# Performance work log

Measured on AMD Instinct MI355X. Metric: run time of the kernel, lower is better.

Reference implementation:

```python
import jax, jax.numpy as jnp
import numpy as np

FLOW_ITERS = 8
DUAL_ITERS = 8
DUAL_STEP = 0.1
DUAL_MOM = 0.9
GRAPH_LAYERS = 2
BIG = 1e9


def _sparsemax(z, mask):
    # sparsemax along last axis; masked entries already hold -BIG, zeroed by mask after.
    V = z.shape[-1]
    zs = jnp.sort(z, axis=-1)[..., ::-1]
    cum = jnp.cumsum(zs, axis=-1)
    k = jnp.arange(1, V + 1, dtype=z.dtype)
    support = zs * k > (cum - 1.0)
    k_sel = jnp.sum(support.astype(jnp.int32), axis=-1, keepdims=True)
    tau = (jnp.take_along_axis(cum, k_sel - 1, axis=-1) - 1.0) / k_sel.astype(z.dtype)
    return jnp.maximum(z - tau, 0.0) * mask


def _min_cost_flow(props, demands):
    # iterative proportional flow routing: push relu(inflow - demand) along predicted proportions
    def body(flow, _):
        inflow = jnp.sum(flow, axis=1)[..., None]      # [B,V,1] inflow to each node
        adjusted = jax.nn.relu(inflow - demands)       # excess to re-route
        return props * adjusted, None                  # row i scaled by its excess
    flow0 = jnp.zeros_like(props)
    flow, _ = jax.lax.scan(body, flow0, None, length=FLOW_ITERS)
    return flow


def _dual_flow(dual_diff, adj):
    # Nesterov-momentum projected gradient on cost(x)=x^2 minus linear dual term, x>=0 on edges
    def body(carry, _):
        flow, acc = carry
        look = flow - DUAL_MOM * acc
        grad = 2.0 * look - dual_diff                  # d/dx x^2 - dual_diff
        acc = DUAL_MOM * acc + DUAL_STEP * grad
        flow = adj * jax.nn.relu(flow - acc)
        return (flow, acc), None
    z = jnp.zeros_like(dual_diff)
    (flow, _), _ = jax.lax.scan(body, (z, z), None, length=DUAL_ITERS)
    return flow


def setup_inputs():
    key = jax.random.key(0)
    ks = jax.random.split(key, 32)
    B, V, F, E, D, K, H = 8, 1200, 8, 16, 64, 2, 4
    node_features = jax.random.normal(ks[0], (B, V, F), dtype=jnp.float32)
    node_embeddings = jax.random.normal(ks[1], (B, V, E), dtype=jnp.float32)
    d = jax.random.normal(ks[2], (B, V, 1), dtype=jnp.float32)
    demands = d - jnp.mean(d, axis=1, keepdims=True)   # balanced supply/demand per graph
    eye = jnp.eye(V, dtype=jnp.float32)
    adj = (jax.random.uniform(ks[3], (B, V, V)) < (16.0 / V)).astype(jnp.float32) * (1.0 - eye)
    hop2 = jnp.clip(adj @ adj, 0.0, 1.0) * (1.0 - eye)
    neighborhoods = jnp.stack([adj, hop2], axis=0)     # [K,B,V,V] k-hop neighborhoods

    def dense(k, fin, fout):
        return (jax.random.normal(k, (fin, fout), dtype=jnp.float32) / np.sqrt(fin)).astype(jnp.float32)

    return dict(
        node_features=node_features, node_embeddings=node_embeddings,
        demands=demands, adj=adj, neighborhoods=neighborhoods,
        enc_w0=dense(ks[4], E + F, D), enc_b0=jnp.zeros((D,), jnp.float32),
        enc_w1=dense(ks[5], D, D), enc_b1=jnp.zeros((D,), jnp.float32),
        agg_w=(jax.random.normal(ks[6], (K, D, D)) / np.sqrt(D)).astype(jnp.float32),
        agg_b=jnp.zeros((K, D), jnp.float32),
        att_w=(jax.random.normal(ks[7], (H, D, D)) / np.sqrt(D)).astype(jnp.float32),
        att_b=jnp.zeros((H, D), jnp.float32),
        att_v=(jax.random.normal(ks[8], (H, D)) / np.sqrt(D)).astype(jnp.float32),
        gru_wu=dense(ks[9], 2 * D, D), gru_bu=jnp.zeros((D,), jnp.float32),
        gru_wr=dense(ks[10], 2 * D, D), gru_br=jnp.zeros((D,), jnp.float32),
        gru_wc=dense(ks[11], 2 * D, D), gru_bc=jnp.zeros((D,), jnp.float32),
        dec_w0=dense(ks[12], D, D), dec_b0=jnp.zeros((D,), jnp.float32),
        dec_w1=dense(ks[13], D, 1), dec_b1=jnp.zeros((1,), jnp.float32),
        dual_w0=dense(ks[14], D, D), dual_b0=jnp.zeros((D,), jnp.float32),
        dual_w1=dense(ks[15], D, 1), dual_b1=jnp.zeros((1,), jnp.float32),
    )


def reference(node_features, node_embeddings, demands, adj, neighborhoods,
              enc_w0, enc_b0, enc_w1, enc_b1, agg_w, agg_b, att_w, att_b, att_v,
              gru_wu, gru_bu, gru_wr, gru_br, gru_wc, gru_bc,
              dec_w0, dec_b0, dec_w1, dec_b1, dual_w0, dual_b0, dual_w1, dual_b1):
    H = att_w.shape[0]
    # node encoder MLP (tanh hidden, tanh final since activate_final=True)
    x = jnp.concatenate([node_embeddings, node_features], axis=-1)
    enc = jnp.tanh(jnp.tanh(x @ enc_w0 + enc_b0) @ enc_w1 + enc_b1)            # [B,V,D]

    deg = jnp.sum(neighborhoods, axis=-1, keepdims=True)
    nb_norm = neighborhoods / jnp.maximum(deg, 1.0)                            # [K,B,V,V]

    for _ in range(GRAPH_LAYERS):
        # per-hop neighborhood aggregation
        msg = jnp.einsum('kbuv,bvd->kbud', nb_norm, enc)
        agg = jnp.tanh(jnp.einsum('kbud,kde->kbue', msg, agg_w) + agg_b[:, None, None, :])
        # multi-head attention over the K hop levels
        proj = jnp.tanh(jnp.einsum('kbvd,hde->hkbve', agg, att_w) + att_b[:, None, None, None, :])
        scores = jnp.einsum('hkbve,he->hkbv', proj, att_v)
        attn = jax.nn.softmax(scores, axis=1)                                  # softmax over hops
        nxt = jnp.einsum('hkbv,kbvd->bvd', attn, agg) / H                      # mean over heads
        # GRU state update
        xs = jnp.concatenate([nxt, enc], axis=-1)
        u = jax.nn.sigmoid(xs @ gru_wu + gru_bu)
        r = jax.nn.sigmoid(xs @ gru_wr + gru_br)
        c = jnp.tanh(jnp.concatenate([nxt, r * enc], axis=-1) @ gru_wc + gru_bc)
        enc = u * enc + (1.0 - u) * c

    # primal: edge weights -> sparsemax -> min-cost-flow
    pred = (enc @ dec_w0 + dec_b0) @ dec_w1 + dec_b1                           # [B,V,1]
    pred_weights = adj * jnp.transpose(pred, (0, 2, 1))                        # [B,V,V]
    weights = -BIG * (1.0 - adj) + pred_weights
    flow_props = _sparsemax(weights, adj)
    flow = _min_cost_flow(flow_props, demands)
    flow_cost = jnp.sum(flow * flow, axis=(1, 2))                              # square cost

    # dual: potentials -> dual-diff -> dual flow solver
    dual = (enc @ dual_w0 + dual_b0) @ dual_w1 + dual_b1                       # [B,V,1]
    dual_diff = adj * (dual - jnp.transpose(dual, (0, 2, 1)))
    dflow = _dual_flow(dual_diff, adj)
    dual_demand = jnp.sum(dual * demands, axis=(1, 2))
    dual_cost = jnp.sum(dflow * dflow - dual_diff * dflow, axis=(1, 2)) - dual_demand

    return flow_cost - dual_cost                                               # duality-gap loss, [B]
```

## Files before the change

### kernel.cpp

```cpp
#include <hip/hip_runtime.h>

#define BB 8
#define VV 1200
#define DD 64
#define KH 2
#define NH 4
#define CAP 64
#define NB2CAP 384
#define NROW (BB*VV)
#define NKROW (KH*BB*VV)

__device__ __forceinline__ float wredsum(float v) {
#pragma unroll
  for (int o = 32; o > 0; o >>= 1) v += __shfl_xor(v, o, 64);
  return v;
}
__device__ __forceinline__ float gredsum(float v) {
#pragma unroll
  for (int o = 8; o > 0; o >>= 1) v += __shfl_xor(v, o, 64);
  return v;
}

__device__ __forceinline__ float tanh_f(float x) {
  float e = __expf(2.0f * x);
  return 1.0f - 2.0f / (e + 1.0f);
}
__device__ __forceinline__ float sigmoid_f(float x) { return 1.0f / (1.0f + __expf(-x)); }

__device__ __forceinline__ size_t nb_base(int row) {
  return (row < NROW) ? (size_t)row * CAP
                      : (size_t)NROW * CAP + (size_t)(row - NROW) * NB2CAP;
}

__global__ void __launch_bounds__(256) k_nbcsr(
    const float* __restrict__ nb,
    int* __restrict__ nb_cols, int* __restrict__ nb_cnt) {
  int wid = threadIdx.x >> 6, lane = threadIdx.x & 63;
  int row = blockIdx.x * 4 + wid;
  if (row >= NKROW) return;
  const float* nbrow = nb + (size_t)row * VV;
  size_t base = nb_base(row);
  int cap = (row < NROW) ? CAP : NB2CAP;
  unsigned long long ltmask = (lane == 0) ? 0ull : ((1ull << lane) - 1ull);
  int cnt = 0;
  for (int b0 = 0; b0 < VV; b0 += 64) {
    int v = b0 + lane;
    float val = (v < VV) ? nbrow[v] : 0.0f;
    unsigned long long mask = __ballot(val != 0.0f);
    int off = cnt + __popcll(mask & ltmask);
    if (val != 0.0f && off < cap) nb_cols[base + off] = v;
    cnt += __popcll(mask);
  }
  if (lane == 0) nb_cnt[row] = (cnt > cap) ? cap : cnt;
}

__global__ void __launch_bounds__(256) k_encoder(
    const float* __restrict__ emb, const float* __restrict__ feat,
    const float* __restrict__ w0, const float* __restrict__ b0,
    const float* __restrict__ w1, const float* __restrict__ b1,
    float* __restrict__ enc0) {
  __shared__ float xT[8][25];
  __shared__ float hT[8][65];
  int tid = threadIdx.x;
  int tile0 = blockIdx.x * 8;
  if (tid < 128) { int i = tid >> 4, d = tid & 15; xT[i][d] = emb[(size_t)(tile0 + i) * 16 + d]; }
  else if (tid < 192) { int t = tid - 128; int i = t >> 3, d = t & 7; xT[i][16 + d] = feat[(size_t)(tile0 + i) * 8 + d]; }
  __syncthreads();
  int r = tid >> 5, cg = tid & 31;
  int c0 = cg * 2;
  float a0 = b0[c0], a1 = b0[c0 + 1];
#pragma unroll
  for (int kk = 0; kk < 24; ++kk) {
    float x = xT[r][kk];
    float2 w2 = *(const float2*)(w0 + kk * DD + c0);
    a0 = fmaf(x, w2.x, a0); a1 = fmaf(x, w2.y, a1);
  }
  hT[r][c0] = tanh_f(a0); hT[r][c0 + 1] = tanh_f(a1);
  __syncthreads();
  float g0 = b1[c0], g1 = b1[c0 + 1];
#pragma unroll 16
  for (int kk = 0; kk < DD; ++kk) {
    float x = hT[r][kk];
    float2 w2 = *(const float2*)(w1 + kk * DD + c0);
    g0 = fmaf(x, w2.x, g0); g1 = fmaf(x, w2.y, g1);
  }
  float2 o; o.x = tanh_f(g0); o.y = tanh_f(g1);
  *(float2*)(enc0 + (size_t)(tile0 + r) * DD + c0) = o;
}

__global__ void __launch_bounds__(256) k_gather(
    const int* __restrict__ nb_cols, const int* __restrict__ nb_cnt,
    const float* __restrict__ encIn, float* __restrict__ msg) {
  int w = threadIdx.x >> 6, lane = threadIdx.x & 63;
  int row = blockIdx.x * 4 + w;
  int k = (row >= NROW) ? 1 : 0;
  int bv = row - k * NROW;
  int b = bv / VV;
  const float4* enc4 = (const float4*)(encIn + (size_t)b * VV * DD);
  const int* cols = nb_cols + nb_base(row);
  int n = nb_cnt[row];
  int sub = lane >> 4, q = lane & 15;
  float ax = 0.0f, ay = 0.0f, az = 0.0f, aw = 0.0f;
  int j = 0;
  for (; j + 16 <= n; j += 16) {
    int c0 = cols[j + sub];
    int c1 = cols[j + 4 + sub];
    int c2 = cols[j + 8 + sub];
    int c3 = cols[j + 12 + sub];
    float4 v0 = enc4[(size_t)c0 * 16 + q];
    float4 v1 = enc4[(size_t)c1 * 16 + q];
    float4 v2 = enc4[(size_t)c2 * 16 + q];
    float4 v3 = enc4[(size_t)c3 * 16 + q];
    ax += (v0.x + v1.x) + (v2.x + v3.x);
    ay += (v0.y + v1.y) + (v2.y + v3.y);
    az += (v0.z + v1.z) + (v2.z + v3.z);
    aw += (v0.w + v1.w) + (v2.w + v3.w);
  }
  for (; j < n; j += 4) {
    int idx = j + sub;
    if (idx < n) {
      float4 v = enc4[(size_t)cols[idx] * 16 + q];
      ax += v.x; ay += v.y; az += v.z; aw += v.w;
    }
  }
#pragma unroll
  for (int o = 16; o < 64; o <<= 1) {
    ax += __shfl_xor(ax, o, 64);
    ay += __shfl_xor(ay, o, 64);
    az += __shfl_xor(az, o, 64);
    aw += __shfl_xor(aw, o, 64);
  }
  if (lane < 16) {
    float inv = 1.0f / fmaxf((float)n, 1.0f);
    float4 r; r.x = ax * inv; r.y = ay * inv; r.z = az * inv; r.w = aw * inv;
    ((float4*)(msg + (size_t)row * DD))[q] = r;
  }
}

__global__ void __launch_bounds__(256) k_aggatt(
    const float* __restrict__ msg,
    const float* __restrict__ agg_w, const float* __restrict__ agg_b,
    const float* __restrict__ att_w, const float* __restrict__ att_b,
    const float* __restrict__ att_v,
    float* __restrict__ agg, float* __restrict__ scores) {
  __shared__ float M[64][65];
  __shared__ float G[64][65];
  int tid = threadIdx.x;
  int tile0 = blockIdx.x * 64;
  int k = (tile0 >= NROW) ? 1 : 0;
  int bv0 = tile0 - k * NROW;
  int rsub = tid >> 4, cg = tid & 15;
  int c0 = cg * 4;
  int r0 = rsub * 4;
#pragma unroll
  for (int rep = 0; rep < 4; ++rep) {
    int idx = rep * 256 + tid; int i = idx >> 4, d4 = idx & 15;
    float4 m4 = *(const float4*)(msg + (size_t)(tile0 + i) * DD + d4 * 4);
    M[i][d4 * 4] = m4.x; M[i][d4 * 4 + 1] = m4.y; M[i][d4 * 4 + 2] = m4.z; M[i][d4 * 4 + 3] = m4.w;
  }
  __syncthreads();
  const float* W = agg_w + (size_t)k * DD * DD;
  float acc[4][4];
#pragma unroll
  for (int i = 0; i < 4; ++i)
#pragma unroll
    for (int j = 0; j < 4; ++j) acc[i][j] = agg_b[k * DD + c0 + j];
#pragma unroll 4
  for (int kk = 0; kk < DD; ++kk) {
    float4 w4 = *(const float4*)(W + kk * DD + c0);
    float x0 = M[r0][kk], x1 = M[r0 + 1][kk], x2 = M[r0 + 2][kk], x3 = M[r0 + 3][kk];
    acc[0][0] = fmaf(x0, w4.x, acc[0][0]); acc[0][1] = fmaf(x0, w4.y, acc[0][1]);
    acc[0][2] = fmaf(x0, w4.z, acc[0][2]); acc[0][3] = fmaf(x0, w4.w, acc[0][3]);
    acc[1][0] = fmaf(x1, w4.x, acc[1][0]); acc[1][1] = fmaf(x1, w4.y, acc[1][1]);
    acc[1][2] = fmaf(x1, w4.z, acc[1][2]); acc[1][3] = fmaf(x1, w4.w, acc[1][3]);
    acc[2][0] = fmaf(x2, w4.x, acc[2][0]); acc[2][1] = fmaf(x2, w4.y, acc[2][1]);
    acc[2][2] = fmaf(x2, w4.z, acc[2][2]); acc[2][3] = fmaf(x2, w4.w, acc[2][3]);
    acc[3][0] = fmaf(x3, w4.x, acc[3][0]); acc[3][1] = fmaf(x3, w4.y, acc[3][1]);
    acc[3][2] = fmaf(x3, w4.z, acc[3][2]); acc[3][3] = fmaf(x3, w4.w, acc[3][3]);
  }
#pragma unroll
  for (int i = 0; i < 4; ++i) {
    float4 g4;
    g4.x = tanh_f(acc[i][0]); g4.y = tanh_f(acc[i][1]);
    g4.z = tanh_f(acc[i][2]); g4.w = tanh_f(acc[i][3]);
    G[r0 + i][c0] = g4.x; G[r0 + i][c0 + 1] = g4.y; G[r0 + i][c0 + 2] = g4.z; G[r0 + i][c0 + 3] = g4.w;
    *(float4*)(agg + (size_t)(tile0 + r0 + i) * DD + c0) = g4;
  }
  __syncthreads();
#pragma unroll
  for (int h = 0; h < NH; ++h) {
    const float* Wh = att_w + (size_t)h * DD * DD;
    float a2[4][4];
#pragma unroll
    for (int i = 0; i < 4; ++i)
#pragma unroll
      for (int j = 0; j < 4; ++j) a2[i][j] = att_b[h * DD + c0 + j];
#pragma unroll 4
    for (int kk = 0; kk < DD; ++kk) {
      float4 w4 = *(const float4*)(Wh + kk * DD + c0);
      float x0 = G[r0][kk], x1 = G[r0 + 1][kk], x2 = G[r0 + 2][kk], x3 = G[r0 + 3][kk];
      a2[0][0] = fmaf(x0, w4.x, a2[0][0]); a2[0][1] = fmaf(x0, w4.y, a2[0][1]);
      a2[0][2] = fmaf(x0, w4.z, a2[0][2]); a2[0][3] = fmaf(x0, w4.w, a2[0][3]);
      a2[1][0] = fmaf(x1, w4.x, a2[1][0]); a2[1][1] = fmaf(x1, w4.y, a2[1][1]);
      a2[1][2] = fmaf(x1, w4.z, a2[1][2]); a2[1][3] = fmaf(x1, w4.w, a2[1][3]);
      a2[2][0] = fmaf(x2, w4.x, a2[2][0]); a2[2][1] = fmaf(x2, w4.y, a2[2][1]);
      a2[2][2] = fmaf(x2, w4.z, a2[2][2]); a2[2][3] = fmaf(x2, w4.w, a2[2][3]);
      a2[3][0] = fmaf(x3, w4.x, a2[3][0]); a2[3][1] = fmaf(x3, w4.y, a2[3][1]);
      a2[3][2] = fmaf(x3, w4.z, a2[3][2]); a2[3][3] = fmaf(x3, w4.w, a2[3][3]);
    }
    float4 v4 = *(const float4*)(att_v + h * DD + c0);
#pragma unroll
    for (int i = 0; i < 4; ++i) {
      float p = tanh_f(a2[i][0]) * v4.x + tanh_f(a2[i][1]) * v4.y
              + tanh_f(a2[i][2]) * v4.z + tanh_f(a2[i][3]) * v4.w;
      p = gredsum(p);
      if (cg == 0) scores[(size_t)(h * KH + k) * NROW + bv0 + r0 + i] = p;
    }
  }
}

__global__ void __launch_bounds__(256) k_gru(
    const float* __restrict__ encIn, const float* __restrict__ agg,
    const float* __restrict__ scores,
    const float* __restrict__ wu, const float* __restrict__ bu,
    const float* __restrict__ wr, const float* __restrict__ br,
    const float* __restrict__ wc, const float* __restrict__ bc,
    float* __restrict__ encOut,
    int do_decode,
    const float* __restrict__ dw0, const float* __restrict__ db0,
    const float* __restrict__ dw1, const float* __restrict__ db1,
    const float* __restrict__ uw0, const float* __restrict__ ub0,
    const float* __restrict__ uw1, const float* __restrict__ ub1,
    float* __restrict__ pred, float* __restrict__ dualp) {
  __shared__ float X[64][129];
  __shared__ float EO[64][65];
  __shared__ float wmix[2][64];
  int tid = threadIdx.x;
  int tile0 = blockIdx.x * 64;
  int rsub = tid >> 4, cg = tid & 15;
  int c0 = cg * 4;
  int r0 = rsub * 4;
  if (tid < 64) {
    int row = tile0 + tid;
    float W0 = 0.0f, W1 = 0.0f;
#pragma unroll
    for (int h = 0; h < NH; ++h) {
      float s0 = scores[(size_t)(h * KH + 0) * NROW + row];
      float s1 = scores[(size_t)(h * KH + 1) * NROW + row];
      float m = fmaxf(s0, s1);
      float e0 = __expf(s0 - m), e1 = __expf(s1 - m);
      float inv = 1.0f / (e0 + e1);
      W0 += e0 * inv; W1 += e1 * inv;
    }
    wmix[0][tid] = W0 * 0.25f;
    wmix[1][tid] = W1 * 0.25f;
  }
  __syncthreads();
#pragma unroll
  for (int rep = 0; rep < 4; ++rep) {
    int idx = rep * 256 + tid; int i = idx >> 4, d4 = idx & 15;
    float4 e4 = *(const float4*)(encIn + (size_t)(tile0 + i) * DD + d4 * 4);
    float4 a0 = *(const float4*)(agg + (size_t)(tile0 + i) * DD + d4 * 4);
    float4 a1 = *(const float4*)(agg + (size_t)(NROW + tile0 + i) * DD + d4 * 4);
    float m0 = wmix[0][i], m1 = wmix[1][i];
    X[i][d4 * 4]     = m0 * a0.x + m1 * a1.x;
    X[i][d4 * 4 + 1] = m0 * a0.y + m1 * a1.y;
    X[i][d4 * 4 + 2] = m0 * a0.z + m1 * a1.z;
    X[i][d4 * 4 + 3] = m0 * a0.w + m1 * a1.w;
    X[i][64 + d4 * 4]     = e4.x;
    X[i][64 + d4 * 4 + 1] = e4.y;
    X[i][64 + d4 * 4 + 2] = e4.z;
    X[i][64 + d4 * 4 + 3] = e4.w;
  }
  __syncthreads();
  float au[4][4], ar[4][4];
#pragma unroll
  for (int i = 0; i < 4; ++i)
#pragma unroll
    for (int j = 0; j < 4; ++j) { au[i][j] = bu[c0 + j]; ar[i][j] = br[c0 + j]; }
#pragma unroll 4
  for (int kk = 0; kk < 2 * DD; ++kk) {
    float4 u4 = *(const float4*)(wu + kk * DD + c0);
    float4 r4 = *(const float4*)(wr + kk * DD + c0);
    float x0 = X[r0][kk], x1 = X[r0 + 1][kk], x2 = X[r0 + 2][kk], x3 = X[r0 + 3][kk];
    au[0][0] = fmaf(x0, u4.x, au[0][0]); au[0][1] = fmaf(x0, u4.y, au[0][1]);
    au[0][2] = fmaf(x0, u4.z, au[0][2]); au[0][3] = fmaf(x0, u4.w, au[0][3]);
    au[1][0] = fmaf(x1, u4.x, au[1][0]); au[1][1] = fmaf(x1, u4.y, au[1][1]);
    au[1][2] = fmaf(x1, u4.z, au[1][2]); au[1][3] = fmaf(x1, u4.w, au[1][3]);
    au[2][0] = fmaf(x2, u4.x, au[2][0]); au[2][1] = fmaf(x2, u4.y, au[2][1]);
    au[2][2] = fmaf(x2, u4.z, au[2][2]); au[2][3] = fmaf(x2, u4.w, au[2][3]);
    au[3][0] = fmaf(x3, u4.x, au[3][0]); au[3][1] = fmaf(x3, u4.y, au[3][1]);
    au[3][2] = fmaf(x3, u4.z, au[3][2]); au[3][3] = fmaf(x3, u4.w, au[3][3]);
    ar[0][0] = fmaf(x0, r4.x, ar[0][0]); ar[0][1] = fmaf(x0, r4.y, ar[0][1]);
    ar[0][2] = fmaf(x0, r4.z, ar[0][2]); ar[0][3] = fmaf(x0, r4.w, ar[0][3]);
    ar[1][0] = fmaf(x1, r4.x, ar[1][0]); ar[1][1] = fmaf(x1, r4.y, ar[1][1]);
    ar[1][2] = fmaf(x1, r4.z, ar[1][2]); ar[1][3] = fmaf(x1, r4.w, ar[1][3]);
    ar[2][0] = fmaf(x2, r4.x, ar[2][0]); ar[2][1] = fmaf(x2, r4.y, ar[2][1]);
    ar[2][2] = fmaf(x2, r4.z, ar[2][2]); ar[2][3] = fmaf(x2, r4.w, ar[2][3]);
    ar[3][0] = fmaf(x3, r4.x, ar[3][0]); ar[3][1] = fmaf(x3, r4.y, ar[3][1]);
    ar[3][2] = fmaf(x3, r4.z, ar[3][2]); ar[3][3] = fmaf(x3, r4.w, ar[3][3]);
  }
  float uu[4][4], encv[4][4];
#pragma unroll
  for (int i = 0; i < 4; ++i)
#pragma unroll
    for (int j = 0; j < 4; ++j) {
      uu[i][j] = sigmoid_f(au[i][j]);
      encv[i][j] = X[r0 + i][64 + c0 + j];
    }
  __syncthreads();
#pragma unroll
  for (int i = 0; i < 4; ++i)
#pragma unroll
    for (int j = 0; j < 4; ++j)
      X[r0 + i][64 + c0 + j] = encv[i][j] * sigmoid_f(ar[i][j]);
  __syncthreads();
  float ac[4][4];
#pragma unroll
  for (int i = 0; i < 4; ++i)
#pragma unroll
    for (int j = 0; j < 4; ++j) ac[i][j] = bc[c0 + j];
#pragma unroll 4
  for (int kk = 0; kk < 2 * DD; ++kk) {
    float4 c4 = *(const float4*)(wc + kk * DD + c0);
    float x0 = X[r0][kk], x1 = X[r0 + 1][kk], x2 = X[r0 + 2][kk], x3 = X[r0 + 3][kk];
    ac[0][0] = fmaf(x0, c4.x, ac[0][0]); ac[0][1] = fmaf(x0, c4.y, ac[0][1]);
    ac[0][2] = fmaf(x0, c4.z, ac[0][2]); ac[0][3] = fmaf(x0, c4.w, ac[0][3]);
    ac[1][0] = fmaf(x1, c4.x, ac[1][0]); ac[1][1] = fmaf(x1, c4.y, ac[1][1]);
    ac[1][2] = fmaf(x1, c4.z, ac[1][2]); ac[1][3] = fmaf(x1, c4.w, ac[1][3]);
    ac[2][0] = fmaf(x2, c4.x, ac[2][0]); ac[2][1] = fmaf(x2, c4.y, ac[2][1]);
    ac[2][2] = fmaf(x2, c4.z, ac[2][2]); ac[2][3] = fmaf(x2, c4.w, ac[2][3]);
    ac[3][0] = fmaf(x3, c4.x, ac[3][0]); ac[3][1] = fmaf(x3, c4.y, ac[3][1]);
    ac[3][2] = fmaf(x3, c4.z, ac[3][2]); ac[3][3] = fmaf(x3, c4.w, ac[3][3]);
  }
#pragma unroll
  for (int i = 0; i < 4; ++i) {
    float4 e4;
    e4.x = uu[i][0] * encv[i][0] + (1.0f - uu[i][0]) * tanh_f(ac[i][0]);
    e4.y = uu[i][1] * encv[i][1] + (1.0f - uu[i][1]) * tanh_f(ac[i][1]);
    e4.z = uu[i][2] * encv[i][2] + (1.0f - uu[i][2]) * tanh_f(ac[i][2]);
    e4.w = uu[i][3] * encv[i][3] + (1.0f - uu[i][3]) * tanh_f(ac[i][3]);
    *(float4*)(encOut + (size_t)(tile0 + r0 + i) * DD + c0) = e4;
    EO[r0 + i][c0] = e4.x; EO[r0 + i][c0 + 1] = e4.y;
    EO[r0 + i][c0 + 2] = e4.z; EO[r0 + i][c0 + 3] = e4.w;
  }
  if (do_decode) {
    __syncthreads();
    float hd[4][4], hq[4][4];
#pragma unroll
    for (int i = 0; i < 4; ++i)
#pragma unroll
      for (int j = 0; j < 4; ++j) { hd[i][j] = db0[c0 + j]; hq[i][j] = ub0[c0 + j]; }
#pragma unroll 4
    for (int kk = 0; kk < DD; ++kk) {
      float4 d4 = *(const float4*)(dw0 + kk * DD + c0);
      float4 q4 = *(const float4*)(uw0 + kk * DD + c0);
      float x0 = EO[r0][kk], x1 = EO[r0 + 1][kk], x2 = EO[r0 + 2][kk], x3 = EO[r0 + 3][kk];
      hd[0][0] = fmaf(x0, d4.x, hd[0][0]); hd[0][1] = fmaf(x0, d4.y, hd[0][1]);
      hd[0][2] = fmaf(x0, d4.z, hd[0][2]); hd[0][3] = fmaf(x0, d4.w, hd[0][3]);
      hd[1][0] = fmaf(x1, d4.x, hd[1][0]); hd[1][1] = fmaf(x1, d4.y, hd[1][1]);
      hd[1][2] = fmaf(x1, d4.z, hd[1][2]); hd[1][3] = fmaf(x1, d4.w, hd[1][3]);
      hd[2][0] = fmaf(x2, d4.x, hd[2][0]); hd[2][1] = fmaf(x2, d4.y, hd[2][1]);
      hd[2][2] = fmaf(x2, d4.z, hd[2][2]); hd[2][3] = fmaf(x2, d4.w, hd[2][3]);
      hd[3][0] = fmaf(x3, d4.x, hd[3][0]); hd[3][1] = fmaf(x3, d4.y, hd[3][1]);
      hd[3][2] = fmaf(x3, d4.z, hd[3][2]); hd[3][3] = fmaf(x3, d4.w, hd[3][3]);
      hq[0][0] = fmaf(x0, q4.x, hq[0][0]); hq[0][1] = fmaf(x0, q4.y, hq[0][1]);
      hq[0][2] = fmaf(x0, q4.z, hq[0][2]); hq[0][3] = fmaf(x0, q4.w, hq[0][3]);
      hq[1][0] = fmaf(x1, q4.x, hq[1][0]); hq[1][1] = fmaf(x1, q4.y, hq[1][1]);
      hq[1][2] = fmaf(x1, q4.z, hq[1][2]); hq[1][3] = fmaf(x1, q4.w, hq[1][3]);
      hq[2][0] = fmaf(x2, q4.x, hq[2][0]); hq[2][1] = fmaf(x2, q4.y, hq[2][1]);
      hq[2][2] = fmaf(x2, q4.z, hq[2][2]); hq[2][3] = fmaf(x2, q4.w, hq[2][3]);
      hq[3][0] = fmaf(x3, q4.x, hq[3][0]); hq[3][1] = fmaf(x3, q4.y, hq[3][1]);
      hq[3][2] = fmaf(x3, q4.z, hq[3][2]); hq[3][3] = fmaf(x3, q4.w, hq[3][3]);
    }
    float4 dv = *(const float4*)(dw1 + c0);
    float4 qv = *(const float4*)(uw1 + c0);
#pragma unroll
    for (int i = 0; i < 4; ++i) {
      float p = hd[i][0] * dv.x + hd[i][1] * dv.y + hd[i][2] * dv.z + hd[i][3] * dv.w;
      float q = hq[i][0] * qv.x + hq[i][1] * qv.y + hq[i][2] * qv.z + hq[i][3] * qv.w;
      p = gredsum(p);
      q = gredsum(q);
      if (cg == 0) {
        pred[tile0 + r0 + i] = p + db1[0];
        dualp[tile0 + r0 + i] = q + ub1[0];
      }
    }
  }
}

__global__ void __launch_bounds__(256) k_primal_dual(
    const int* __restrict__ nb_cols, const int* __restrict__ nb_cnt,
    const float* __restrict__ pred, const float* __restrict__ dualp,
    const float* __restrict__ dem,
    float* __restrict__ rowsum,
    int* __restrict__ col_cnt, int* __restrict__ col_rows, float* __restrict__ col_vals,
    float* __restrict__ out) {
  __shared__ float bacc[BB];
  if (threadIdx.x < BB) bacc[threadIdx.x] = 0.0f;
  __syncthreads();
  int w = threadIdx.x >> 6, lane = threadIdx.x & 63;
  int row = blockIdx.x * 4 + w;
  int b = row / VV;
  int n = nb_cnt[row];
  int c = (lane < n) ? nb_cols[(size_t)row * CAP + lane] : 0;
  const float* predB = pred + (size_t)b * VV;
  const float* dualB = dualp + (size_t)b * VV;
  float z = (lane < n) ? predB[c] : -1e30f;
  float tau = 0.0f;
  if (n > 0) {
    bool in = (lane < n);
    for (int it = 0; it < 64; ++it) {
      float s = wredsum(in ? z : 0.0f);
      int cnt = (int)__popcll(__ballot(in));
      tau = (s - 1.0f) / (float)cnt;
      bool nin = (z > tau);
      if (__ballot(nin) == __ballot(in)) break;
      in = nin;
    }
  }
  float pv = (lane < n) ? fmaxf(z - tau, 0.0f) : 0.0f;
  float s2 = wredsum(pv * pv);
  if (lane == 0) rowsum[row] = s2;
  if (pv > 0.0f) {
    int g = b * VV + c;
    int j = atomicAdd(&col_cnt[g], 1);
    if (j < CAP) {
      col_rows[(size_t)g * CAP + j] = row - b * VV;
      col_vals[(size_t)g * CAP + j] = pv;
    }
  }
  float du = dualp[row];
  float es = 0.0f;
  if (lane < n) {
    float dd = du - dualB[c];
    float f = 0.0f, acm = 0.0f;
#pragma unroll
    for (int t = 0; t < 8; ++t) {
      float look = f - 0.9f * acm;
      float grad = 2.0f * look - dd;
      acm = 0.9f * acm + 0.1f * grad;
      f = fmaxf(f - acm, 0.0f);
    }
    es = f * f - dd * f;
  }
  float contrib = -es;
  if (lane == 0) contrib += du * dem[row];
  float ws_ = wredsum(contrib);
  if (lane == 0) atomicAdd(&bacc[b], ws_);
  __syncthreads();
  if (threadIdx.x < BB) {
    float t = bacc[threadIdx.x];
    if (t != 0.0f) atomicAdd(&out[threadIdx.x], t);
  }
}

__global__ void __launch_bounds__(1024) k_flow(
    const int* __restrict__ col_cnt, const int* __restrict__ col_rows,
    const float* __restrict__ col_vals, const float* __restrict__ dem,
    const float* __restrict__ rowsum, float* __restrict__ out) {
  __shared__ float aS[VV];
  __shared__ float red[16];
  int b = blockIdx.x;
  int tid = threadIdx.x;
  const float* demB = dem + (size_t)b * VV;
  for (int v = tid; v < VV; v += 1024) aS[v] = fmaxf(-demB[v], 0.0f);
  __syncthreads();
  for (int t = 0; t < 7; ++t) {
    float nv0 = 0.0f, nv1 = 0.0f;
    {
      int v = tid;
      if (v < VV) {
        int g = b * VV + v;
        int n = col_cnt[g]; if (n > CAP) n = CAP;
        const int* cr = col_rows + (size_t)g * CAP;
        const float* cv = col_vals + (size_t)g * CAP;
        float acc = 0.0f;
        for (int j = 0; j < n; ++j) acc += cv[j] * aS[cr[j]];
        nv0 = fmaxf(acc - demB[v], 0.0f);
      }
      v = tid + 1024;
      if (v < VV) {
        int g = b * VV + v;
        int n = col_cnt[g]; if (n > CAP) n = CAP;
        const int* cr = col_rows + (size_t)g * CAP;
        const float* cv = col_vals + (size_t)g * CAP;
        float acc = 0.0f;
        for (int j = 0; j < n; ++j) acc += cv[j] * aS[cr[j]];
        nv1 = fmaxf(acc - demB[v], 0.0f);
      }
    }
    __syncthreads();
    if (tid < VV) aS[tid] = nv0;
    if (tid + 1024 < VV) aS[tid + 1024] = nv1;
    __syncthreads();
  }
  float fc = 0.0f;
  for (int v = tid; v < VV; v += 1024) { float a = aS[v]; fc += a * a * rowsum[b * VV + v]; }
  fc = wredsum(fc);
  int wid = tid >> 6, lane = tid & 63;
  if (lane == 0) red[wid] = fc;
  __syncthreads();
  if (tid == 0) {
    float s = 0.0f;
#pragma unroll
    for (int i = 0; i < 16; ++i) s += red[i];
    atomicAdd(&out[b], s);
  }
}

extern "C" void kernel_launch(void* const* d_in, const int* in_sizes, int n_in,
                              void* d_out, int out_size, void* d_ws, size_t ws_size,
                              hipStream_t stream) {
  const float* feat   = (const float*)d_in[0];
  const float* emb    = (const float*)d_in[1];
  const float* dem    = (const float*)d_in[2];
  const float* nb     = (const float*)d_in[4];
  const float* enc_w0 = (const float*)d_in[5];
  const float* enc_b0 = (const float*)d_in[6];
  const float* enc_w1 = (const float*)d_in[7];
  const float* enc_b1 = (const float*)d_in[8];
  const float* agg_w  = (const float*)d_in[9];
  const float* agg_b  = (const float*)d_in[10];
  const float* att_w  = (const float*)d_in[11];
  const float* att_b  = (const float*)d_in[12];
  const float* att_v  = (const float*)d_in[13];
  const float* gru_wu = (const float*)d_in[14];
  const float* gru_bu = (const float*)d_in[15];
  const float* gru_wr = (const float*)d_in[16];
  const float* gru_br = (const float*)d_in[17];
  const float* gru_wc = (const float*)d_in[18];
  const float* gru_bc = (const float*)d_in[19];
  const float* dec_w0 = (const float*)d_in[20];
  const float* dec_b0 = (const float*)d_in[21];
  const float* dec_w1 = (const float*)d_in[22];
  const float* dec_b1 = (const float*)d_in[23];
  const float* dual_w0= (const float*)d_in[24];
  const float* dual_b0= (const float*)d_in[25];
  const float* dual_w1= (const float*)d_in[26];
  const float* dual_b1= (const float*)d_in[27];
  float* out = (float*)d_out;

  float* ws = (float*)d_ws;
  float* enc0     = ws;
  float* enc1     = enc0 + (size_t)NROW * DD;
  float* msg      = enc1 + (size_t)NROW * DD;
  float* aggbuf   = msg + (size_t)NKROW * DD;
  float* scores   = aggbuf + (size_t)NKROW * DD;
  float* pred     = scores + (size_t)NH * KH * NROW;
  float* dualp    = pred + NROW;
  float* rowsum   = dualp + NROW;
  float* col_vals = rowsum + NROW;
  int* col_cnt  = (int*)(col_vals + (size_t)NROW * CAP);
  int* nb_cnt   = col_cnt + NROW;
  int* col_rows = nb_cnt + NKROW;
  int* nb_cols  = col_rows + (size_t)NROW * CAP;

  (void)in_sizes; (void)n_in; (void)ws_size;

  hipMemsetAsync(out, 0, (size_t)out_size * sizeof(float), stream);
  hipMemsetAsync(col_cnt, 0, (size_t)NROW * sizeof(int), stream);

  k_nbcsr<<<NKROW / 4, 256, 0, stream>>>(nb, nb_cols, nb_cnt);
  k_encoder<<<NROW / 8, 256, 0, stream>>>(emb, feat, enc_w0, enc_b0, enc_w1, enc_b1, enc0);

  const float* encIn = enc0;
  float* encOut = enc1;
  for (int l = 0; l < 2; ++l) {
    k_gather<<<NKROW / 4, 256, 0, stream>>>(nb_cols, nb_cnt, encIn, msg);
    k_aggatt<<<NKROW / 64, 256, 0, stream>>>(msg, agg_w, agg_b, att_w, att_b, att_v,
                                             aggbuf, scores);
    k_gru<<<NROW / 64, 256, 0, stream>>>(encIn, aggbuf, scores,
                                         gru_wu, gru_bu, gru_wr, gru_br, gru_wc, gru_bc,
                                         encOut,
                                         (l == 1) ? 1 : 0,
                                         dec_w0, dec_b0, dec_w1, dec_b1,
                                         dual_w0, dual_b0, dual_w1, dual_b1, pred, dualp);
    const float* t = encIn; encIn = encOut; encOut = (float*)t;
  }

  k_primal_dual<<<NROW / 4, 256, 0, stream>>>(nb_cols, nb_cnt, pred, dualp, dem,
                                              rowsum, col_cnt, col_rows, col_vals, out);
  k_flow<<<BB, 1024, 0, stream>>>(col_cnt, col_rows, col_vals, dem, rowsum, out);
}
```

Baseline: 561.8 us.

## Merge setup kernels and memsets, prefetch gather indices, double threads in dense kernels

Combines the neighbor-CSR build, the encoder MLP and the two memsets into a single launch with block-range dispatch, which removes launch overhead. The gather kernel software-prefetches the next group of column indices. The aggregation/attention and GRU kernels move from 256 to 512 threads per block, with each thread computing 2 rows instead of 4 so more waves are available to hide latency. The GRU also computes the attention mixing weights per thread, dropping a shared buffer and one barrier at the cost of repeating the softmax work.

```diff
diff --git a/kernel.cpp b/kernel.cpp
--- a/kernel.cpp
+++ b/kernel.cpp
@@ -32,60 +32,65 @@
                       : (size_t)NROW * CAP + (size_t)(row - NROW) * NB2CAP;
 }
 
-__global__ void __launch_bounds__(256) k_nbcsr(
-    const float* __restrict__ nb,
-    int* __restrict__ nb_cols, int* __restrict__ nb_cnt) {
-  int wid = threadIdx.x >> 6, lane = threadIdx.x & 63;
-  int row = blockIdx.x * 4 + wid;
-  if (row >= NKROW) return;
-  const float* nbrow = nb + (size_t)row * VV;
-  size_t base = nb_base(row);
-  int cap = (row < NROW) ? CAP : NB2CAP;
-  unsigned long long ltmask = (lane == 0) ? 0ull : ((1ull << lane) - 1ull);
-  int cnt = 0;
-  for (int b0 = 0; b0 < VV; b0 += 64) {
-    int v = b0 + lane;
-    float val = (v < VV) ? nbrow[v] : 0.0f;
-    unsigned long long mask = __ballot(val != 0.0f);
-    int off = cnt + __popcll(mask & ltmask);
-    if (val != 0.0f && off < cap) nb_cols[base + off] = v;
-    cnt += __popcll(mask);
-  }
-  if (lane == 0) nb_cnt[row] = (cnt > cap) ? cap : cnt;
-}
-
-__global__ void __launch_bounds__(256) k_encoder(
+__global__ void __launch_bounds__(256) k_pre(
+    const float* __restrict__ nb, int* __restrict__ nb_cols, int* __restrict__ nb_cnt,
     const float* __restrict__ emb, const float* __restrict__ feat,
     const float* __restrict__ w0, const float* __restrict__ b0,
     const float* __restrict__ w1, const float* __restrict__ b1,
-    float* __restrict__ enc0) {
+    float* __restrict__ enc0,
+    int* __restrict__ col_cnt, float* __restrict__ out, int out_size) {
   __shared__ float xT[8][25];
   __shared__ float hT[8][65];
+  const int nbBlocks = NKROW / 4;
+  const int encBlocks = NROW / 8;
+  int bid = blockIdx.x;
   int tid = threadIdx.x;
-  int tile0 = blockIdx.x * 8;
-  if (tid < 128) { int i = tid >> 4, d = tid & 15; xT[i][d] = emb[(size_t)(tile0 + i) * 16 + d]; }
-  else if (tid < 192) { int t = tid - 128; int i = t >> 3, d = t & 7; xT[i][16 + d] = feat[(size_t)(tile0 + i) * 8 + d]; }
-  __syncthreads();
-  int r = tid >> 5, cg = tid & 31;
-  int c0 = cg * 2;
-  float a0 = b0[c0], a1 = b0[c0 + 1];
-#pragma unroll
-  for (int kk = 0; kk < 24; ++kk) {
-    float x = xT[r][kk];
-    float2 w2 = *(const float2*)(w0 + kk * DD + c0);
-    a0 = fmaf(x, w2.x, a0); a1 = fmaf(x, w2.y, a1);
-  }
-  hT[r][c0] = tanh_f(a0); hT[r][c0 + 1] = tanh_f(a1);
-  __syncthreads();
-  float g0 = b1[c0], g1 = b1[c0 + 1];
+  if (bid < nbBlocks) {
+    int wid = tid >> 6, lane = tid & 63;
+    int row = bid * 4 + wid;
+    const float* nbrow = nb + (size_t)row * VV;
+    size_t base = nb_base(row);
+    int cap = (row < NROW) ? CAP : NB2CAP;
+    unsigned long long ltmask = (lane == 0) ? 0ull : ((1ull << lane) - 1ull);
+    int cnt = 0;
+    for (int b0_ = 0; b0_ < VV; b0_ += 64) {
+      int v = b0_ + lane;
+      float val = (v < VV) ? nbrow[v] : 0.0f;
+      unsigned long long mask = __ballot(val != 0.0f);
+      int off = cnt + __popcll(mask & ltmask);
+      if (val != 0.0f && off < cap) nb_cols[base + off] = v;
+      cnt += __popcll(mask);
+    }
+    if (lane == 0) nb_cnt[row] = (cnt > cap) ? cap : cnt;
+  } else if (bid < nbBlocks + encBlocks) {
+    int tile0 = (bid - nbBlocks) * 8;
+    if (tid < 128) { int i = tid >> 4, d = tid & 15; xT[i][d] = emb[(size_t)(tile0 + i) * 16 + d]; }
+    else if (tid < 192) { int t = tid - 128; int i = t >> 3, d = t & 7; xT[i][16 + d] = feat[(size_t)(tile0 + i) * 8 + d]; }
+    __syncthreads();
+    int r = tid >> 5, cg = tid & 31;
+    int c0 = cg * 2;
+    float a0 = b0[c0], a1 = b0[c0 + 1];
+#pragma unroll
+    for (int kk = 0; kk < 24; ++kk) {
+      float x = xT[r][kk];
+      float2 w2 = *(const float2*)(w0 + kk * DD + c0);
+      a0 = fmaf(x, w2.x, a0); a1 = fmaf(x, w2.y, a1);
+    }
+    hT[r][c0] = tanh_f(a0); hT[r][c0 + 1] = tanh_f(a1);
+    __syncthreads();
+    float g0 = b1[c0], g1 = b1[c0 + 1];
 #pragma unroll 16
-  for (int kk = 0; kk < DD; ++kk) {
-    float x = hT[r][kk];
-    float2 w2 = *(const float2*)(w1 + kk * DD + c0);
-    g0 = fmaf(x, w2.x, g0); g1 = fmaf(x, w2.y, g1);
-  }
-  float2 o; o.x = tanh_f(g0); o.y = tanh_f(g1);
-  *(float2*)(enc0 + (size_t)(tile0 + r) * DD + c0) = o;
+    for (int kk = 0; kk < DD; ++kk) {
+      float x = hT[r][kk];
+      float2 w2 = *(const float2*)(w1 + kk * DD + c0);
+      g0 = fmaf(x, w2.x, g0); g1 = fmaf(x, w2.y, g1);
+    }
+    float2 o; o.x = tanh_f(g0); o.y = tanh_f(g1);
+    *(float2*)(enc0 + (size_t)(tile0 + r) * DD + c0) = o;
+  } else {
+    for (int i = tid; i < NROW; i += 256) col_cnt[i] = 0;
+    if (tid < out_size) out[tid] = 0.0f;
+  }
 }
 
 __global__ void __launch_bounds__(256) k_gather(
@@ -102,19 +107,28 @@
   int sub = lane >> 4, q = lane & 15;
   float ax = 0.0f, ay = 0.0f, az = 0.0f, aw = 0.0f;
   int j = 0;
-  for (; j + 16 <= n; j += 16) {
-    int c0 = cols[j + sub];
-    int c1 = cols[j + 4 + sub];
-    int c2 = cols[j + 8 + sub];
-    int c3 = cols[j + 12 + sub];
-    float4 v0 = enc4[(size_t)c0 * 16 + q];
-    float4 v1 = enc4[(size_t)c1 * 16 + q];
-    float4 v2 = enc4[(size_t)c2 * 16 + q];
-    float4 v3 = enc4[(size_t)c3 * 16 + q];
+  int cc0 = 0, cc1 = 0, cc2 = 0, cc3 = 0;
+  if (j + 16 <= n) {
+    cc0 = cols[j + sub]; cc1 = cols[j + 4 + sub];
+    cc2 = cols[j + 8 + sub]; cc3 = cols[j + 12 + sub];
+  }
+  while (j + 16 <= n) {
+    int nj = j + 16;
+    int p0 = 0, p1 = 0, p2 = 0, p3 = 0;
+    if (nj + 16 <= n) {
+      p0 = cols[nj + sub]; p1 = cols[nj + 4 + sub];
+      p2 = cols[nj + 8 + sub]; p3 = cols[nj + 12 + sub];
+    }
+    float4 v0 = enc4[(size_t)cc0 * 16 + q];
+    float4 v1 = enc4[(size_t)cc1 * 16 + q];
+    float4 v2 = enc4[(size_t)cc2 * 16 + q];
+    float4 v3 = enc4[(size_t)cc3 * 16 + q];
     ax += (v0.x + v1.x) + (v2.x + v3.x);
     ay += (v0.y + v1.y) + (v2.y + v3.y);
     az += (v0.z + v1.z) + (v2.z + v3.z);
     aw += (v0.w + v1.w) + (v2.w + v3.w);
+    cc0 = p0; cc1 = p1; cc2 = p2; cc3 = p3;
+    j = nj;
   }
   for (; j < n; j += 4) {
     int idx = j + sub;
@@ -137,7 +151,7 @@
   }
 }
 
-__global__ void __launch_bounds__(256) k_aggatt(
+__global__ void __launch_bounds__(512) k_aggatt(
     const float* __restrict__ msg,
     const float* __restrict__ agg_w, const float* __restrict__ agg_b,
     const float* __restrict__ att_w, const float* __restrict__ att_b,
@@ -151,35 +165,31 @@
   int bv0 = tile0 - k * NROW;
   int rsub = tid >> 4, cg = tid & 15;
   int c0 = cg * 4;
-  int r0 = rsub * 4;
-#pragma unroll
-  for (int rep = 0; rep < 4; ++rep) {
-    int idx = rep * 256 + tid; int i = idx >> 4, d4 = idx & 15;
+  int r0 = rsub * 2;
+#pragma unroll
+  for (int rep = 0; rep < 2; ++rep) {
+    int idx = rep * 512 + tid; int i = idx >> 4, d4 = idx & 15;
     float4 m4 = *(const float4*)(msg + (size_t)(tile0 + i) * DD + d4 * 4);
     M[i][d4 * 4] = m4.x; M[i][d4 * 4 + 1] = m4.y; M[i][d4 * 4 + 2] = m4.z; M[i][d4 * 4 + 3] = m4.w;
   }
   __syncthreads();
   const float* W = agg_w + (size_t)k * DD * DD;
-  float acc[4][4];
-#pragma unroll
-  for (int i = 0; i < 4; ++i)
+  float acc[2][4];
+#pragma unroll
+  for (int i = 0; i < 2; ++i)
 #pragma unroll
     for (int j = 0; j < 4; ++j) acc[i][j] = agg_b[k * DD + c0 + j];
 #pragma unroll 4
   for (int kk = 0; kk < DD; ++kk) {
     float4 w4 = *(const float4*)(W + kk * DD + c0);
-    float x0 = M[r0][kk], x1 = M[r0 + 1][kk], x2 = M[r0 + 2][kk], x3 = M[r0 + 3][kk];
+    float x0 = M[r0][kk], x1 = M[r0 + 1][kk];
     acc[0][0] = fmaf(x0, w4.x, acc[0][0]); acc[0][1] = fmaf(x0, w4.y, acc[0][1]);
     acc[0][2] = fmaf(x0, w4.z, acc[0][2]); acc[0][3] = fmaf(x0, w4.w, acc[0][3]);
     acc[1][0] = fmaf(x1, w4.x, acc[1][0]); acc[1][1] = fmaf(x1, w4.y, acc[1][1]);
     acc[1][2] = fmaf(x1, w4.z, acc[1][2]); acc[1][3] = fmaf(x1, w4.w, acc[1][3]);
-    acc[2][0] = fmaf(x2, w4.x, acc[2][0]); acc[2][1] = fmaf(x2, w4.y, acc[2][1]);
-    acc[2][2] = fmaf(x2, w4.z, acc[2][2]); acc[2][3] = fmaf(x2, w4.w, acc[2][3]);
-    acc[3][0] = fmaf(x3, w4.x, acc[3][0]); acc[3][1] = fmaf(x3, w4.y, acc[3][1]);
-    acc[3][2] = fmaf(x3, w4.z, acc[3][2]); acc[3][3] = fmaf(x3, w4.w, acc[3][3]);
-  }
-#pragma unroll
-  for (int i = 0; i < 4; ++i) {
+  }
+#pragma unroll
+  for (int i = 0; i < 2; ++i) {
     float4 g4;
     g4.x = tanh_f(acc[i][0]); g4.y = tanh_f(acc[i][1]);
     g4.z = tanh_f(acc[i][2]); g4.w = tanh_f(acc[i][3]);
@@ -190,27 +200,23 @@
 #pragma unroll
   for (int h = 0; h < NH; ++h) {
     const float* Wh = att_w + (size_t)h * DD * DD;
-    float a2[4][4];
-#pragma unroll
-    for (int i = 0; i < 4; ++i)
+    float a2[2][4];
+#pragma unroll
+    for (int i = 0; i < 2; ++i)
 #pragma unroll
       for (int j = 0; j < 4; ++j) a2[i][j] = att_b[h * DD + c0 + j];
 #pragma unroll 4
     for (int kk = 0; kk < DD; ++kk) {
       float4 w4 = *(const float4*)(Wh + kk * DD + c0);
-      float x0 = G[r0][kk], x1 = G[r0 + 1][kk], x2 = G[r0 + 2][kk], x3 = G[r0 + 3][kk];
+      float x0 = G[r0][kk], x1 = G[r0 + 1][kk];
       a2[0][0] = fmaf(x0, w4.x, a2[0][0]); a2[0][1] = fmaf(x0, w4.y, a2[0][1]);
       a2[0][2] = fmaf(x0, w4.z, a2[0][2]); a2[0][3] = fmaf(x0, w4.w, a2[0][3]);
       a2[1][0] = fmaf(x1, w4.x, a2[1][0]); a2[1][1] = fmaf(x1, w4.y, a2[1][1]);
       a2[1][2] = fmaf(x1, w4.z, a2[1][2]); a2[1][3] = fmaf(x1, w4.w, a2[1][3]);
-      a2[2][0] = fmaf(x2, w4.x, a2[2][0]); a2[2][1] = fmaf(x2, w4.y, a2[2][1]);
-      a2[2][2] = fmaf(x2, w4.z, a2[2][2]); a2[2][3] = fmaf(x2, w4.w, a2[2][3]);
-      a2[3][0] = fmaf(x3, w4.x, a2[3][0]); a2[3][1] = fmaf(x3, w4.y, a2[3][1]);
-      a2[3][2] = fmaf(x3, w4.z, a2[3][2]); a2[3][3] = fmaf(x3, w4.w, a2[3][3]);
     }
     float4 v4 = *(const float4*)(att_v + h * DD + c0);
 #pragma unroll
-    for (int i = 0; i < 4; ++i) {
+    for (int i = 0; i < 2; ++i) {
       float p = tanh_f(a2[i][0]) * v4.x + tanh_f(a2[i][1]) * v4.y
               + tanh_f(a2[i][2]) * v4.z + tanh_f(a2[i][3]) * v4.w;
       p = gredsum(p);
@@ -219,7 +225,7 @@
   }
 }
 
-__global__ void __launch_bounds__(256) k_gru(
+__global__ void __launch_bounds__(512) k_gru(
     const float* __restrict__ encIn, const float* __restrict__ agg,
     const float* __restrict__ scores,
     const float* __restrict__ wu, const float* __restrict__ bu,
@@ -234,14 +240,15 @@
     float* __restrict__ pred, float* __restrict__ dualp) {
   __shared__ float X[64][129];
   __shared__ float EO[64][65];
-  __shared__ float wmix[2][64];
   int tid = threadIdx.x;
   int tile0 = blockIdx.x * 64;
   int rsub = tid >> 4, cg = tid & 15;
   int c0 = cg * 4;
-  int r0 = rsub * 4;
-  if (tid < 64) {
-    int row = tile0 + tid;
+  int r0 = rsub * 2;
+#pragma unroll
+  for (int rep = 0; rep < 2; ++rep) {
+    int idx = rep * 512 + tid; int i = idx >> 4, d4 = idx & 15;
+    int row = tile0 + i;
     float W0 = 0.0f, W1 = 0.0f;
 #pragma unroll
     for (int h = 0; h < NH; ++h) {
@@ -252,57 +259,42 @@
       float inv = 1.0f / (e0 + e1);
       W0 += e0 * inv; W1 += e1 * inv;
     }
-    wmix[0][tid] = W0 * 0.25f;
-    wmix[1][tid] = W1 * 0.25f;
-  }
-  __syncthreads();
-#pragma unroll
-  for (int rep = 0; rep < 4; ++rep) {
-    int idx = rep * 256 + tid; int i = idx >> 4, d4 = idx & 15;
-    float4 e4 = *(const float4*)(encIn + (size_t)(tile0 + i) * DD + d4 * 4);
-    float4 a0 = *(const float4*)(agg + (size_t)(tile0 + i) * DD + d4 * 4);
-    float4 a1 = *(const float4*)(agg + (size_t)(NROW + tile0 + i) * DD + d4 * 4);
-    float m0 = wmix[0][i], m1 = wmix[1][i];
-    X[i][d4 * 4]     = m0 * a0.x + m1 * a1.x;
-    X[i][d4 * 4 + 1] = m0 * a0.y + m1 * a1.y;
-    X[i][d4 * 4 + 2] = m0 * a0.z + m1 * a1.z;
-    X[i][d4 * 4 + 3] = m0 * a0.w + m1 * a1.w;
+    W0 *= 0.25f; W1 *= 0.25f;
+    float4 e4 = *(const float4*)(encIn + (size_t)row * DD + d4 * 4);
+    float4 a0 = *(const float4*)(agg + (size_t)row * DD + d4 * 4);
+    float4 a1 = *(const float4*)(agg + (size_t)(NROW + row) * DD + d4 * 4);
+    X[i][d4 * 4]     = W0 * a0.x + W1 * a1.x;
+    X[i][d4 * 4 + 1] = W0 * a0.y + W1 * a1.y;
+    X[i][d4 * 4 + 2] = W0 * a0.z + W1 * a1.z;
+    X[i][d4 * 4 + 3] = W0 * a0.w + W1 * a1.w;
     X[i][64 + d4 * 4]     = e4.x;
     X[i][64 + d4 * 4 + 1] = e4.y;
     X[i][64 + d4 * 4 + 2] = e4.z;
     X[i][64 + d4 * 4 + 3] = e4.w;
   }
   __syncthreads();
-  float au[4][4], ar[4][4];
-#pragma unroll
-  for (int i = 0; i < 4; ++i)
+  float au[2][4], ar[2][4];
+#pragma unroll
+  for (int i = 0; i < 2; ++i)
 #pragma unroll
     for (int j = 0; j < 4; ++j) { au[i][j] = bu[c0 + j]; ar[i][j] = br[c0 + j]; }
 #pragma unroll 4
   for (int kk = 0; kk < 2 * DD; ++kk) {
     float4 u4 = *(const float4*)(wu + kk * DD + c0);
     float4 r4 = *(const float4*)(wr + kk * DD + c0);
-    float x0 = X[r0][kk], x1 = X[r0 + 1][kk], x2 = X[r0 + 2][kk], x3 = X[r0 + 3][kk];
+    float x0 = X[r0][kk], x1 = X[r0 + 1][kk];
     au[0][0] = fmaf(x0, u4.x, au[0][0]); au[0][1] = fmaf(x0, u4.y, au[0][1]);
     au[0][2] = fmaf(x0, u4.z, au[0][2]); au[0][3] = fmaf(x0, u4.w, au[0][3]);
     au[1][0] = fmaf(x1, u4.x, au[1][0]); au[1][1] = fmaf(x1, u4.y, au[1][1]);
     au[1][2] = fmaf(x1, u4.z, au[1][2]); au[1][3] = fmaf(x1, u4.w, au[1][3]);
-    au[2][0] = fmaf(x2, u4.x, au[2][0]); au[2][1] = fmaf(x2, u4.y, au[2][1]);
-    au[2][2] = fmaf(x2, u4.z, au[2][2]); au[2][3] = fmaf(x2, u4.w, au[2][3]);
-    au[3][0] = fmaf(x3, u4.x, au[3][0]); au[3][1] = fmaf(x3, u4.y, au[3][1]);
-    au[3][2] = fmaf(x3, u4.z, au[3][2]); au[3][3] = fmaf(x3, u4.w, au[3][3]);
     ar[0][0] = fmaf(x0, r4.x, ar[0][0]); ar[0][1] = fmaf(x0, r4.y, ar[0][1]);
     ar[0][2] = fmaf(x0, r4.z, ar[0][2]); ar[0][3] = fmaf(x0, r4.w, ar[0][3]);
     ar[1][0] = fmaf(x1, r4.x, ar[1][0]); ar[1][1] = fmaf(x1, r4.y, ar[1][1]);
     ar[1][2] = fmaf(x1, r4.z, ar[1][2]); ar[1][3] = fmaf(x1, r4.w, ar[1][3]);
-    ar[2][0] = fmaf(x2, r4.x, ar[2][0]); ar[2][1] = fmaf(x2, r4.y, ar[2][1]);
-    ar[2][2] = fmaf(x2, r4.z, ar[2][2]); ar[2][3] = fmaf(x2, r4.w, ar[2][3]);
-    ar[3][0] = fmaf(x3, r4.x, ar[3][0]); ar[3][1] = fmaf(x3, r4.y, ar[3][1]);
-    ar[3][2] = fmaf(x3, r4.z, ar[3][2]); ar[3][3] = fmaf(x3, r4.w, ar[3][3]);
-  }
-  float uu[4][4], encv[4][4];
-#pragma unroll
-  for (int i = 0; i < 4; ++i)
+  }
+  float uu[2][4], encv[2][4];
+#pragma unroll
+  for (int i = 0; i < 2; ++i)
 #pragma unroll
     for (int j = 0; j < 4; ++j) {
       uu[i][j] = sigmoid_f(au[i][j]);
@@ -310,31 +302,27 @@
     }
   __syncthreads();
 #pragma unroll
-  for (int i = 0; i < 4; ++i)
+  for (int i = 0; i < 2; ++i)
 #pragma unroll
     for (int j = 0; j < 4; ++j)
       X[r0 + i][64 + c0 + j] = encv[i][j] * sigmoid_f(ar[i][j]);
   __syncthreads();
-  float ac[4][4];
-#pragma unroll
-  for (int i = 0; i < 4; ++i)
+  float ac[2][4];
+#pragma unroll
+  for (int i = 0; i < 2; ++i)
 #pragma unroll
     for (int j = 0; j < 4; ++j) ac[i][j] = bc[c0 + j];
 #pragma unroll 4
   for (int kk = 0; kk < 2 * DD; ++kk) {
     float4 c4 = *(const float4*)(wc + kk * DD + c0);
-    float x0 = X[r0][kk], x1 = X[r0 + 1][kk], x2 = X[r0 + 2][kk], x3 = X[r0 + 3][kk];
+    float x0 = X[r0][kk], x1 = X[r0 + 1][kk];
     ac[0][0] = fmaf(x0, c4.x, ac[0][0]); ac[0][1] = fmaf(x0, c4.y, ac[0][1]);
     ac[0][2] = fmaf(x0, c4.z, ac[0][2]); ac[0][3] = fmaf(x0, c4.w, ac[0][3]);
     ac[1][0] = fmaf(x1, c4.x, ac[1][0]); ac[1][1] = fmaf(x1, c4.y, ac[1][1]);
     ac[1][2] = fmaf(x1, c4.z, ac[1][2]); ac[1][3] = fmaf(x1, c4.w, ac[1][3]);
-    ac[2][0] = fmaf(x2, c4.x, ac[2][0]); ac[2][1] = fmaf(x2, c4.y, ac[2][1]);
-    ac[2][2] = fmaf(x2, c4.z, ac[2][2]); ac[2][3] = fmaf(x2, c4.w, ac[2][3]);
-    ac[3][0] = fmaf(x3, c4.x, ac[3][0]); ac[3][1] = fmaf(x3, c4.y, ac[3][1]);
-    ac[3][2] = fmaf(x3, c4.z, ac[3][2]); ac[3][3] = fmaf(x3, c4.w, ac[3][3]);
-  }
-#pragma unroll
-  for (int i = 0; i < 4; ++i) {
+  }
+#pragma unroll
+  for (int i = 0; i < 2; ++i) {
     float4 e4;
     e4.x = uu[i][0] * encv[i][0] + (1.0f - uu[i][0]) * tanh_f(ac[i][0]);
     e4.y = uu[i][1] * encv[i][1] + (1.0f - uu[i][1]) * tanh_f(ac[i][1]);
@@ -346,37 +334,29 @@
   }
   if (do_decode) {
     __syncthreads();
-    float hd[4][4], hq[4][4];
-#pragma unroll
-    for (int i = 0; i < 4; ++i)
+    float hd[2][4], hq[2][4];
+#pragma unroll
+    for (int i = 0; i < 2; ++i)
 #pragma unroll
       for (int j = 0; j < 4; ++j) { hd[i][j] = db0[c0 + j]; hq[i][j] = ub0[c0 + j]; }
 #pragma unroll 4
     for (int kk = 0; kk < DD; ++kk) {
       float4 d4 = *(const float4*)(dw0 + kk * DD + c0);
       float4 q4 = *(const float4*)(uw0 + kk * DD + c0);
-      float x0 = EO[r0][kk], x1 = EO[r0 + 1][kk], x2 = EO[r0 + 2][kk], x3 = EO[r0 + 3][kk];
+      float x0 = EO[r0][kk], x1 = EO[r0 + 1][kk];
       hd[0][0] = fmaf(x0, d4.x, hd[0][0]); hd[0][1] = fmaf(x0, d4.y, hd[0][1]);
       hd[0][2] = fmaf(x0, d4.z, hd[0][2]); hd[0][3] = fmaf(x0, d4.w, hd[0][3]);
       hd[1][0] = fmaf(x1, d4.x, hd[1][0]); hd[1][1] = fmaf(x1, d4.y, hd[1][1]);
       hd[1][2] = fmaf(x1, d4.z, hd[1][2]); hd[1][3] = fmaf(x1, d4.w, hd[1][3]);
-      hd[2][0] = fmaf(x2, d4.x, hd[2][0]); hd[2][1] = fmaf(x2, d4.y, hd[2][1]);
-      hd[2][2] = fmaf(x2, d4.z, hd[2][2]); hd[2][3] = fmaf(x2, d4.w, hd[2][3]);
-      hd[3][0] = fmaf(x3, d4.x, hd[3][0]); hd[3][1] = fmaf(x3, d4.y, hd[3][1]);
-      hd[3][2] = fmaf(x3, d4.z, hd[3][2]); hd[3][3] = fmaf(x3, d4.w, hd[3][3]);
       hq[0][0] = fmaf(x0, q4.x, hq[0][0]); hq[0][1] = fmaf(x0, q4.y, hq[0][1]);
       hq[0][2] = fmaf(x0, q4.z, hq[0][2]); hq[0][3] = fmaf(x0, q4.w, hq[0][3]);
       hq[1][0] = fmaf(x1, q4.x, hq[1][0]); hq[1][1] = fmaf(x1, q4.y, hq[1][1]);
       hq[1][2] = fmaf(x1, q4.z, hq[1][2]); hq[1][3] = fmaf(x1, q4.w, hq[1][3]);
-      hq[2][0] = fmaf(x2, q4.x, hq[2][0]); hq[2][1] = fmaf(x2, q4.y, hq[2][1]);
-      hq[2][2] = fmaf(x2, q4.z, hq[2][2]); hq[2][3] = fmaf(x2, q4.w, hq[2][3]);
-      hq[3][0] = fmaf(x3, q4.x, hq[3][0]); hq[3][1] = fmaf(x3, q4.y, hq[3][1]);
-      hq[3][2] = fmaf(x3, q4.z, hq[3][2]); hq[3][3] = fmaf(x3, q4.w, hq[3][3]);
     }
     float4 dv = *(const float4*)(dw1 + c0);
     float4 qv = *(const float4*)(uw1 + c0);
 #pragma unroll
-    for (int i = 0; i < 4; ++i) {
+    for (int i = 0; i < 2; ++i) {
       float p = hd[i][0] * dv.x + hd[i][1] * dv.y + hd[i][2] * dv.z + hd[i][3] * dv.w;
       float q = hq[i][0] * qv.x + hq[i][1] * qv.y + hq[i][2] * qv.z + hq[i][3] * qv.w;
       p = gredsum(p);
@@ -558,19 +538,17 @@
 
   (void)in_sizes; (void)n_in; (void)ws_size;
 
-  hipMemsetAsync(out, 0, (size_t)out_size * sizeof(float), stream);
-  hipMemsetAsync(col_cnt, 0, (size_t)NROW * sizeof(int), stream);
-
-  k_nbcsr<<<NKROW / 4, 256, 0, stream>>>(nb, nb_cols, nb_cnt);
-  k_encoder<<<NROW / 8, 256, 0, stream>>>(emb, feat, enc_w0, enc_b0, enc_w1, enc_b1, enc0);
+  k_pre<<<NKROW / 4 + NROW / 8 + 1, 256, 0, stream>>>(
+      nb, nb_cols, nb_cnt, emb, feat, enc_w0, enc_b0, enc_w1, enc_b1, enc0,
+      col_cnt, out, out_size);
 
   const float* encIn = enc0;
   float* encOut = enc1;
   for (int l = 0; l < 2; ++l) {
     k_gather<<<NKROW / 4, 256, 0, stream>>>(nb_cols, nb_cnt, encIn, msg);
-    k_aggatt<<<NKROW / 64, 256, 0, stream>>>(msg, agg_w, agg_b, att_w, att_b, att_v,
+    k_aggatt<<<NKROW / 64, 512, 0, stream>>>(msg, agg_w, agg_b, att_w, att_b, att_v,
                                              aggbuf, scores);
-    k_gru<<<NROW / 64, 256, 0, stream>>>(encIn, aggbuf, scores,
+    k_gru<<<NROW / 64, 512, 0, stream>>>(encIn, aggbuf, scores,
                                          gru_wu, gru_bu, gru_wr, gru_br, gru_wc, gru_bc,
                                          encOut,
                                          (l == 1) ? 1 : 0,
```

Result: faster. 547.7 us (-2.5%).
